# Kernel tuning notes

Measured on AMD Instinct MI355X. Metric: run time of the kernel, lower is better.

Reference implementation:

```python
import jax, jax.numpy as jnp
import numpy as np

N, K, D, H, DK, DV, L, E = 16384, 16, 128, 8, 16, 16, 2, 32
DFF = 4 * D
EPS = 1e-5


def _ln(x, g, b):
    mu = jnp.mean(x, axis=-1, keepdims=True)
    var = jnp.var(x, axis=-1, keepdims=True)
    return (x - mu) * jax.lax.rsqrt(var + EPS) * g + b


def setup_inputs() -> dict:
    key = jax.random.key(0)
    ks = jax.random.split(key, 20)
    inp = {
        "node_h": jax.random.normal(ks[0], (N, D), jnp.float32),
        "src_idx": jax.random.randint(ks[1], (N, K), 0, N),
        "edge_feat": jax.random.normal(ks[2], (N, K, E), jnp.float32),
        "t": jax.random.uniform(ks[3], (N, K), jnp.float32),
        "t_now": jnp.ones((1,), jnp.float32),
        # params (linear weights stored [in, out])
        "edge_fc_w": jax.random.normal(ks[4], (E, D), jnp.float32) * (2.0 / (E + D)) ** 0.5,
        "edge_fc_b": jnp.zeros((D,), jnp.float32),
        "basis_freq": jnp.asarray(1.0 / 10 ** np.linspace(0, 9, D), jnp.float32),
        "phase": jax.random.normal(ks[5], (D,), jnp.float32),
        "wq": jax.random.normal(ks[6], (L, D, H * DK), jnp.float32) * np.sqrt(2.0 / (D + DK)),
        "wk": jax.random.normal(ks[7], (L, D, H * DK), jnp.float32) * np.sqrt(2.0 / (D + DK)),
        "wv": jax.random.normal(ks[8], (L, D, H * DV), jnp.float32) * np.sqrt(2.0 / (D + DV)),
        "attn_fc_w": jax.random.normal(ks[9], (L, H * DV, D), jnp.float32) * (2.0 / (H * DV + D)) ** 0.5,
        "attn_fc_b": jnp.zeros((L, D), jnp.float32),
        "attn_ln_g": jnp.ones((L, D), jnp.float32),
        "attn_ln_b": jnp.zeros((L, D), jnp.float32),
        "ffn_w1": jax.random.normal(ks[10], (L, D, DFF), jnp.float32) * (1.0 / D) ** 0.5,
        "ffn_b1": jnp.zeros((L, DFF), jnp.float32),
        "ffn_w2": jax.random.normal(ks[11], (L, DFF, D), jnp.float32) * (1.0 / DFF) ** 0.5,
        "ffn_b2": jnp.zeros((L, D), jnp.float32),
        "ffn_ln_g": jnp.ones((L, D), jnp.float32),
        "ffn_ln_b": jnp.zeros((L, D), jnp.float32),
        "fea2node_w": jax.random.normal(ks[12], (D, D), jnp.float32) * (2.0 / (D + D)) ** 0.5,
        "fea2node_b": jnp.zeros((D,), jnp.float32),
        "final_ln_g": jnp.ones((D,), jnp.float32),
        "final_ln_b": jnp.zeros((D,), jnp.float32),
    }
    return inp


def reference(node_h, src_idx, edge_feat, t, t_now,
              edge_fc_w, edge_fc_b, basis_freq, phase,
              wq, wk, wv, attn_fc_w, attn_fc_b, attn_ln_g, attn_ln_b,
              ffn_w1, ffn_b1, ffn_w2, ffn_b2, ffn_ln_g, ffn_ln_b,
              fea2node_w, fea2node_b, final_ln_g, final_ln_b):
    scale = 1.0 / np.sqrt(DK).astype(np.float32)
    # message_func: gather src features, edge transform, temporal encoding
    t_enc = jnp.cos((t_now[0] - t)[..., None] * basis_freq + phase)        # [N,K,D]
    z = node_h[src_idx] + jax.nn.gelu(edge_feat @ edge_fc_w + edge_fc_b) + t_enc
    # reduce_func: inner_layer transformer blocks over the K-neighbor mailbox
    f = z
    for i in range(L):
        q = (f @ wq[i]).reshape(N, K, H, DK)
        k = (f @ wk[i]).reshape(N, K, H, DK)
        v = (f @ wv[i]).reshape(N, K, H, DV)
        attn = jax.nn.softmax(jnp.einsum('nqhd,nkhd->nhqk', q, k) * scale, axis=-1)
        out = jnp.einsum('nhqk,nkhd->nqhd', attn, v).reshape(N, K, H * DV)
        f = _ln(out @ attn_fc_w[i] + attn_fc_b[i] + f, attn_ln_g[i], attn_ln_b[i])
        hid = jax.nn.relu(f @ ffn_w1[i] + ffn_b1[i])                        # [N,K,4D]
        f = _ln(hid @ ffn_w2[i] + ffn_b2[i] + f, ffn_ln_g[i], ffn_ln_b[i])
    pooled = jnp.mean(f, axis=1)                                            # [N,D]
    out = _ln(jax.nn.gelu(pooled @ fea2node_w + fea2node_b) + node_h,
              final_ln_g, final_ln_b)
    return out
```

## Files before the change

### kernel.cpp

```cpp
#include <hip/hip_runtime.h>

#define NN 16384
#define OFF_EWT 0
#define OFF_WQT 4096
#define OFF_WKT 36864
#define OFF_WVT 69632
#define OFF_AFT 102400
#define OFF_W1T 135168
#define OFF_W2T 266240
#define OFF_F2N 397312
#define TOTAL_W 413696
#define FB_BYTE_OFF (1 << 20)

typedef __attribute__((ext_vector_type(8))) short bf16x8;
typedef __attribute__((ext_vector_type(4))) short bf16x4;
typedef __attribute__((ext_vector_type(4))) float f32x4;

static __device__ __forceinline__ short f2bf(float f) {
  unsigned u = __builtin_bit_cast(unsigned, f);
  u += 0x7fffu + ((u >> 16) & 1u);
  return (short)(u >> 16);
}
static __device__ __forceinline__ float bf2f(short h) {
  unsigned u = ((unsigned)(unsigned short)h) << 16;
  return __builtin_bit_cast(float, u);
}
static __device__ __forceinline__ float gelu_f(float x) {
  float e = __expf(1.5957691216057308f * (x + 0.044715f * x * x * x));
  return x - x / (e + 1.0f);
}
static __device__ __forceinline__ f32x4 mfma16(bf16x8 a, bf16x8 b, f32x4 c) {
  return __builtin_amdgcn_mfma_f32_16x16x32_bf16(a, b, c, 0, 0, 0);
}
#define SWZM(row) (((((row) & 7) << 4)) ^ ((((row) >> 3) & 3) << 5))
static __device__ __forceinline__ int swzb(int row, int col) {
  return row * 256 + ((col * 2) ^ SWZM(row));
}
static __device__ __forceinline__ bf16x8 tile_ld8(const short* base, int row, int col) {
  return *(const bf16x8*)((const char*)base + swzb(row, col));
}
static __device__ __forceinline__ void tile_st16(short* base, int row, int col, short v) {
  *(short*)((char*)base + swzb(row, col)) = v;
}
static __device__ __forceinline__ float tile_ldf(const short* base, int row, int col) {
  return bf2f(*(const short*)((const char*)base + swzb(row, col)));
}
static __device__ __forceinline__ void gll16(const short* sp, void* dstb) {
  __builtin_amdgcn_global_load_lds(
      (const __attribute__((address_space(1))) unsigned int*)sp,
      (__attribute__((address_space(3))) unsigned int*)dstb, 16, 0, 0);
}
static __device__ __forceinline__ void stage8(short* dst, const short* src, int stride,
                                              int w, int lane) {
  int dbase = w * 1024;
  int d = dbase + lane * 16;
  int row = d >> 8;
  int scolb = (d & 255) ^ SWZM(row);
  gll16(src + row * stride + (scolb >> 1), (char*)dst + dbase);
}
static __device__ __forceinline__ void stage_h8(short* dst, const short* src, int stride,
                                                int w, int lane) {
  #pragma unroll
  for (int it = 0; it < 2; ++it) {
    int dbase = (it * 8 + w) * 1024;
    int d = dbase + lane * 16;
    int row = d >> 8;
    int scolb = (d & 255) ^ SWZM(row);
    gll16(src + row * stride + (scolb >> 1), (char*)dst + dbase);
  }
}
static __device__ __forceinline__ void stage_f(short* dst, const short* src, int lane) {
  #pragma unroll
  for (int it = 0; it < 4; ++it) {
    int dbase = it * 1024;
    int d = dbase + lane * 16;
    int row = d >> 8;
    int scolb = (d & 255) ^ SWZM(row);
    gll16(src + row * 128 + (scolb >> 1), (char*)dst + dbase);
  }
}

#define LDS_FENCE() do {                                       \
    asm volatile("s_waitcnt lgkmcnt(0)" ::: "memory");         \
    __builtin_amdgcn_sched_barrier(0);                         \
  } while (0)

#define ENDSTEP() do {                                         \
    __syncthreads();                                           \
    short* _t = bc; bc = bn; bn = _t;                          \
  } while (0)

#define LD_FA(SRC)                                                        \
  _Pragma("unroll") for (int _s = 0; _s < 4; ++_s)                        \
      fA[_s] = tile_ld8((SRC), li, _s * 32 + lq * 8);

#define ST_TILE(T, ACC)                                                   \
  _Pragma("unroll") for (int _c = 0; _c < 8; ++_c)                        \
    _Pragma("unroll") for (int _r = 0; _r < 4; ++_r)                      \
      tile_st16((T), lq * 4 + _r, _c * 16 + li, f2bf((ACC)[_c][_r]));

#define PROJ1(BB)                                                         \
    f32x4 g0 = F0, g1 = F0;                                               \
    _Pragma("unroll") for (int _s = 0; _s < 4; ++_s) {                    \
      int _sc = _s * 32 + lq * 8;                                         \
      bf16x8 _b0 = tile_ld8((BB), 0 + li, _sc);                           \
      bf16x8 _b1 = tile_ld8((BB), 16 + li, _sc);                          \
      g0 = mfma16(fA[_s], _b0, g0);                                       \
      g1 = mfma16(fA[_s], _b1, g1);                                       \
    }

#define ST1(DST, CB)                                                      \
    _Pragma("unroll") for (int _r = 0; _r < 4; ++_r) {                    \
      tile_st16((DST), lq * 4 + _r, (CB) * 16 + li, f2bf(g0[_r]));        \
      tile_st16((DST), lq * 4 + _r, ((CB) + 1) * 16 + li, f2bf(g1[_r]));  \
    }

#define ACC1(AR, CB, BB)                                                  \
    _Pragma("unroll") for (int _s = 0; _s < 4; ++_s) {                    \
      int _sc = _s * 32 + lq * 8;                                         \
      bf16x8 _b0 = tile_ld8((BB), 0 + li, _sc);                           \
      bf16x8 _b1 = tile_ld8((BB), 16 + li, _sc);                          \
      acc[(CB)] = mfma16(AR[_s], _b0, acc[(CB)]);                         \
      acc[(CB) + 1] = mfma16(AR[_s], _b1, acc[(CB) + 1]);                 \
    }

#define PROJ4H(BB)                                                        \
    f32x4 g0 = F0, g1 = F0, g2 = F0, g3 = F0;                             \
    _Pragma("unroll") for (int _s = 0; _s < 4; ++_s) {                    \
      int _sc = _s * 32 + lq * 8;                                         \
      g0 = mfma16(fA[_s], tile_ld8((BB), 0 + li, _sc), g0);               \
      g1 = mfma16(fA[_s], tile_ld8((BB), 16 + li, _sc), g1);              \
      g2 = mfma16(fA[_s], tile_ld8((BB), 32 + li, _sc), g2);              \
      g3 = mfma16(fA[_s], tile_ld8((BB), 48 + li, _sc), g3);              \
    }

#define ACC4H(AR, CB, BB)                                                 \
    _Pragma("unroll") for (int _s = 0; _s < 4; ++_s) {                    \
      int _sc = _s * 32 + lq * 8;                                         \
      acc[(CB) + 0] = mfma16(AR[_s], tile_ld8((BB), 0 + li, _sc), acc[(CB) + 0]);  \
      acc[(CB) + 1] = mfma16(AR[_s], tile_ld8((BB), 16 + li, _sc), acc[(CB) + 1]); \
      acc[(CB) + 2] = mfma16(AR[_s], tile_ld8((BB), 32 + li, _sc), acc[(CB) + 2]); \
      acc[(CB) + 3] = mfma16(AR[_s], tile_ld8((BB), 48 + li, _sc), acc[(CB) + 3]); \
    }

#define LAYER_NORM(A, GP, BP) do {                                        \
    float _gg[8], _bb[8];                                                 \
    _Pragma("unroll") for (int _c = 0; _c < 8; ++_c) {                    \
      _gg[_c] = (GP)[_c * 16 + li]; _bb[_c] = (BP)[_c * 16 + li]; }       \
    _Pragma("unroll") for (int _r = 0; _r < 4; ++_r) {                    \
      float _s1 = 0.f, _s2 = 0.f;                                         \
      _Pragma("unroll") for (int _c = 0; _c < 8; ++_c) {                  \
        float _v = (A)[_c][_r]; _s1 += _v; _s2 += _v * _v; }              \
      _Pragma("unroll") for (int _m = 1; _m <= 8; _m <<= 1) {             \
        _s1 += __shfl_xor(_s1, _m, 64); _s2 += __shfl_xor(_s2, _m, 64); } \
      float _mean = _s1 * (1.f / 128.f);                                  \
      float _var = _s2 * (1.f / 128.f) - _mean * _mean;                   \
      float _rstd = rsqrtf(_var + 1e-5f);                                 \
      _Pragma("unroll") for (int _c = 0; _c < 8; ++_c)                    \
        (A)[_c][_r] = ((A)[_c][_r] - _mean) * _rstd * _gg[_c] + _bb[_c];  \
    }                                                                     \
  } while (0)

#define ATTN(MYQ, MYK, VACC, OA) do {                                     \
    f32x4 _st[8];                                                         \
    _Pragma("unroll") for (int _h = 0; _h < 8; ++_h) {                    \
      bf16x8 _ka = B0, _qa = B0;                                          \
      if (lq < 2) {                                                       \
        _ka = tile_ld8((MYK), li, _h * 16 + lq * 8);                      \
        _qa = tile_ld8((MYQ), li, _h * 16 + lq * 8);                      \
      }                                                                   \
      _st[_h] = mfma16(_ka, _qa, F0);                                     \
    }                                                                     \
    LDS_FENCE();                                                          \
    _Pragma("unroll") for (int _c = 0; _c < 8; ++_c) {                    \
      bf16x4 _pk;                                                         \
      _Pragma("unroll") for (int _r = 0; _r < 4; ++_r)                    \
        _pk[_r] = f2bf((VACC)[_c][_r]);                                   \
      *(bf16x4*)((MYK) + (_c * 16 + li) * 16 + lq * 4) = _pk;             \
    }                                                                     \
    LDS_FENCE();                                                          \
    _Pragma("unroll") for (int _h = 0; _h < 8; ++_h) {                    \
      float _p[4]; float _mx = -1e30f;                                    \
      _Pragma("unroll") for (int _r = 0; _r < 4; ++_r) {                  \
        _p[_r] = _st[_h][_r] * 0.25f; _mx = fmaxf(_mx, _p[_r]); }         \
      _mx = fmaxf(_mx, __shfl_xor(_mx, 16, 64));                          \
      _mx = fmaxf(_mx, __shfl_xor(_mx, 32, 64));                          \
      float _sum = 0.f;                                                   \
      _Pragma("unroll") for (int _r = 0; _r < 4; ++_r) {                  \
        _p[_r] = __expf(_p[_r] - _mx); _sum += _p[_r]; }                  \
      _sum += __shfl_xor(_sum, 16, 64);                                   \
      _sum += __shfl_xor(_sum, 32, 64);                                   \
      float _inv = 1.0f / _sum;                                           \
      _Pragma("unroll") for (int _r = 0; _r < 4; ++_r) _p[_r] *= _inv;    \
      bf16x8 _pa;                                                         \
      _Pragma("unroll") for (int _j = 0; _j < 8; ++_j) {                  \
        float _v = __shfl(_p[_j & 3], li + 16 * (2 * lq + (_j >> 2)), 64);\
        _pa[_j] = (lq < 2) ? f2bf(_v) : (short)0;                         \
      }                                                                   \
      bf16x8 _vb = B0;                                                    \
      if (lq < 2) _vb = *(const bf16x8*)((MYK) + (_h * 16 + li) * 16 + lq * 8); \
      f32x4 _o = mfma16(_pa, _vb, F0);                                    \
      _Pragma("unroll") for (int _r = 0; _r < 4; ++_r)                    \
        tile_st16((MYQ), lq * 4 + _r, _h * 16 + li, f2bf(_o[_r]));        \
    }                                                                     \
    LDS_FENCE();                                                          \
    _Pragma("unroll") for (int _s = 0; _s < 4; ++_s)                      \
      (OA)[_s] = tile_ld8((MYQ), li, _s * 32 + lq * 8);                   \
  } while (0)

__global__ void prep_kernel(const float* __restrict__ ew, const float* __restrict__ wq,
                            const float* __restrict__ wk, const float* __restrict__ wv,
                            const float* __restrict__ afc, const float* __restrict__ w1,
                            const float* __restrict__ w2, const float* __restrict__ f2n,
                            short* __restrict__ wsb) {
  int tt = blockIdx.x * 256 + threadIdx.x;
  if (tt >= TOTAL_W) return;
  short v;
  if (tt < OFF_WQT) {
    int u = tt; int row = u >> 5, colr = u & 31;
    v = f2bf(ew[colr * 128 + row]);
  } else if (tt < OFF_WKT) {
    int u = tt - OFF_WQT; int i = u >> 14; u &= 16383; int row = u >> 7, colr = u & 127;
    v = f2bf(wq[i * 16384 + colr * 128 + row]);
  } else if (tt < OFF_WVT) {
    int u = tt - OFF_WKT; int i = u >> 14; u &= 16383; int row = u >> 7, colr = u & 127;
    v = f2bf(wk[i * 16384 + colr * 128 + row]);
  } else if (tt < OFF_AFT) {
    int u = tt - OFF_WVT; int i = u >> 14; u &= 16383; int row = u >> 7, colr = u & 127;
    v = f2bf(wv[i * 16384 + colr * 128 + row]);
  } else if (tt < OFF_W1T) {
    int u = tt - OFF_AFT; int i = u >> 14; u &= 16383; int row = u >> 7, colr = u & 127;
    v = f2bf(afc[i * 16384 + colr * 128 + row]);
  } else if (tt < OFF_W2T) {
    int u = tt - OFF_W1T; int i = u >> 16; u &= 65535; int row = u >> 7, colr = u & 127;
    v = f2bf(w1[i * 65536 + colr * 512 + row]);
  } else if (tt < OFF_F2N) {
    int u = tt - OFF_W2T; int i = u >> 16; u &= 65535; int row = u >> 9, colr = u & 511;
    v = f2bf(w2[i * 65536 + colr * 128 + row]);
  } else {
    int u = tt - OFF_F2N; int row = u >> 7, colr = u & 127;
    v = f2bf(f2n[colr * 128 + row]);
  }
  wsb[tt] = v;
}

__global__ __launch_bounds__(512, 3) void attn_kernel(
    const float* __restrict__ node_h, const int* __restrict__ src_idx,
    const float* __restrict__ edge_feat, const float* __restrict__ t_arr,
    const float* __restrict__ t_now, const float* __restrict__ edge_fc_b,
    const float* __restrict__ basis_freq, const float* __restrict__ phase,
    const float* __restrict__ attn_fc_b, const float* __restrict__ attn_ln_g,
    const float* __restrict__ attn_ln_b, const short* __restrict__ wsb,
    short* __restrict__ fbuf, int il, int do_msg) {
  __shared__ __align__(16) short bufs0[4096];
  __shared__ __align__(16) short bufs1[4096];
  __shared__ __align__(16) short qk[8][4096];

  const int tid = (int)threadIdx.x;
  const int w = tid >> 6, lane = tid & 63, li = lane & 15, lq = lane >> 4;
  const int n = (int)blockIdx.x * 8 + w;
  short* myQ = qk[w];
  short* myK = qk[w] + 2048;
  short* bc = bufs0;
  short* bn = bufs1;
  const f32x4 F0 = {0.f, 0.f, 0.f, 0.f};
  const bf16x8 B0 = {0, 0, 0, 0, 0, 0, 0, 0};
  const short* WQT = wsb + OFF_WQT + il * 16384;
  const short* WKT = wsb + OFF_WKT + il * 16384;
  const short* WVT = wsb + OFF_WVT + il * 16384;
  const short* AFT = wsb + OFF_AFT + il * 16384;

  stage8(bc, WQT, 128, w, lane);

  f32x4 acc[8];
  if (do_msg) {
    const float tnow = t_now[0];
    {
      const float* ef = edge_feat + ((size_t)(n * 16 + li)) * 32 + lq * 8;
      f32x4 e0 = *(const f32x4*)(ef);
      f32x4 e1 = *(const f32x4*)(ef + 4);
      bf16x8 ea;
      #pragma unroll
      for (int j = 0; j < 4; ++j) { ea[j] = f2bf(e0[j]); ea[j + 4] = f2bf(e1[j]); }
      const short* ewt = wsb + OFF_EWT;
      #pragma unroll
      for (int c = 0; c < 8; ++c) {
        bf16x8 eb = *(const bf16x8*)(ewt + (c * 16 + li) * 32 + lq * 8);
        acc[c] = mfma16(ea, eb, F0);
      }
    }
    {
      float bfq[8], phs[8], ebs[8];
      #pragma unroll
      for (int c = 0; c < 8; ++c) {
        int col = c * 16 + li;
        bfq[c] = basis_freq[col]; phs[c] = phase[col]; ebs[c] = edge_fc_b[col];
      }
      #pragma unroll
      for (int r = 0; r < 4; ++r) {
        int m = lq * 4 + r;
        int sidx = src_idx[n * 16 + m];
        float dt = tnow - t_arr[n * 16 + m];
        const float* nh = node_h + (size_t)sidx * 128;
        #pragma unroll
        for (int c = 0; c < 8; ++c) {
          int col = c * 16 + li;
          float x = gelu_f(acc[c][r] + ebs[c]);
          x += nh[col];
          x += __cosf(dt * bfq[c] + phs[c]);
          acc[c][r] = x;
        }
      }
    }
    ST_TILE(myQ, acc);
  } else {
    stage_f(myQ, fbuf + (size_t)n * 2048, lane);
  }
  __syncthreads();
  if (!do_msg) {
    #pragma unroll
    for (int c = 0; c < 8; ++c)
      #pragma unroll
      for (int r = 0; r < 4; ++r)
        acc[c][r] = tile_ldf(myQ, lq * 4 + r, c * 16 + li);
  }

  bf16x8 fA[4], oa_[4];

  #pragma unroll
  for (int q = 0; q < 4; ++q) {
    const short* nx = (q < 3) ? (WQT + (q + 1) * 4096) : WKT;
    stage8(bn, nx, 128, w, lane);
    if (q == 0) LD_FA(myQ);
    { PROJ1(bc); ST1(myQ, q * 2); }
    ENDSTEP();
  }
  #pragma unroll
  for (int q = 0; q < 4; ++q) {
    const short* nx = (q < 3) ? (WKT + (q + 1) * 4096) : WVT;
    stage8(bn, nx, 128, w, lane);
    { PROJ1(bc); ST1(myK, q * 2); }
    ENDSTEP();
  }
  {
    f32x4 vacc[8];
    #pragma unroll
    for (int q = 0; q < 4; ++q) {
      const short* nx = (q < 3) ? (WVT + (q + 1) * 4096) : AFT;
      stage8(bn, nx, 128, w, lane);
      { PROJ1(bc); vacc[q * 2] = g0; vacc[q * 2 + 1] = g1; }
      if (q == 3) {
        LDS_FENCE();
        ATTN(myQ, myK, vacc, oa_);
      }
      ENDSTEP();
    }
  }
  #pragma unroll
  for (int q = 0; q < 4; ++q) {
    if (q < 3) stage8(bn, AFT + (q + 1) * 4096, 128, w, lane);
    #pragma unroll
    for (int j = 0; j < 2; ++j) {
      float b = attn_fc_b[il * 128 + (q * 2 + j) * 16 + li];
      #pragma unroll
      for (int r = 0; r < 4; ++r) acc[q * 2 + j][r] += b;
    }
    ACC1(oa_, q * 2, bc);
    if (q == 3) {
      LAYER_NORM(acc, attn_ln_g + il * 128, attn_ln_b + il * 128);
      ST_TILE(myQ, acc);
    }
    ENDSTEP();
  }
  LDS_FENCE();
  #pragma unroll
  for (int j = 0; j < 4; ++j) {
    int row = lane >> 2, colb = (lane & 3) * 32 + j * 8;
    bf16x8 v = tile_ld8(myQ, row, colb);
    *(bf16x8*)(fbuf + (size_t)n * 2048 + row * 128 + colb) = v;
  }
}

__global__ __launch_bounds__(512, 2) void ffn_kernel(
    const float* __restrict__ ffn_b1, const float* __restrict__ ffn_b2,
    const float* __restrict__ ffn_ln_g, const float* __restrict__ ffn_ln_b,
    const float* __restrict__ f2n_b, const float* __restrict__ fin_g,
    const float* __restrict__ fin_b, const float* __restrict__ node_h,
    const short* __restrict__ wsb, short* __restrict__ fbuf,
    float* __restrict__ out, int il, int last) {
  __shared__ __align__(16) short bufs0[8192];
  __shared__ __align__(16) short bufs1[8192];
  __shared__ __align__(16) short qk[8][2048];

  const int tid = (int)threadIdx.x;
  const int w = tid >> 6, lane = tid & 63, li = lane & 15, lq = lane >> 4;
  const int n = (int)blockIdx.x * 8 + w;
  short* myK = qk[w];
  short* bc = bufs0;
  short* bn = bufs1;
  const f32x4 F0 = {0.f, 0.f, 0.f, 0.f};
  const short* W1T = wsb + OFF_W1T + il * 65536;
  const short* W2T = wsb + OFF_W2T + il * 65536;

  stage_h8(bc, W1T, 128, w, lane);
  stage_f(myK, fbuf + (size_t)n * 2048, lane);
  __syncthreads();

  bf16x8 fA[4], ha_[4];
  LD_FA(myK);
  f32x4 acc[8];
  #pragma unroll
  for (int c = 0; c < 8; ++c) {
    float b2 = ffn_b2[il * 128 + c * 16 + li];
    #pragma unroll
    for (int r = 0; r < 4; ++r)
      acc[c][r] = tile_ldf(myK, lq * 4 + r, c * 16 + li) + b2;
  }
  LDS_FENCE();

  for (int ct = 0; ct < 4; ++ct) {
    const short* W1c = W1T + ct * 16384;
    const short* W2c = W2T + ct * 128;
    const float* b1p = ffn_b1 + il * 512 + ct * 128;
    #pragma unroll
    for (int h = 0; h < 2; ++h) {
      const short* nx = (h == 0) ? (W1c + 64 * 128) : W2c;
      stage_h8(bn, nx, (h == 0) ? 128 : 512, w, lane);
      {
        PROJ4H(bc);
        #pragma unroll
        for (int j = 0; j < 4; ++j) {
          float b1 = b1p[(h * 4 + j) * 16 + li];
          f32x4 gx = j == 0 ? g0 : j == 1 ? g1 : j == 2 ? g2 : g3;
          #pragma unroll
          for (int r = 0; r < 4; ++r)
            tile_st16(myK, lq * 4 + r, (h * 4 + j) * 16 + li, f2bf(fmaxf(gx[r] + b1, 0.f)));
        }
      }
      if (h == 1) {
        LDS_FENCE();
        #pragma unroll
        for (int s = 0; s < 4; ++s) ha_[s] = tile_ld8(myK, li, s * 32 + lq * 8);
      }
      ENDSTEP();
    }
    #pragma unroll
    for (int h = 0; h < 2; ++h) {
      if (h == 0) stage_h8(bn, W2c + 64 * 512, 512, w, lane);
      else if (ct < 3) stage_h8(bn, W1T + (ct + 1) * 16384, 128, w, lane);
      ACC4H(ha_, h * 4, bc);
      if (ct == 3 && h == 1)
        LAYER_NORM(acc, ffn_ln_g + il * 128, ffn_ln_b + il * 128);
      ENDSTEP();
    }
  }

  if (last) {
    float pc[8];
    #pragma unroll
    for (int c = 0; c < 8; ++c) {
      float s = acc[c][0] + acc[c][1] + acc[c][2] + acc[c][3];
      s += __shfl_xor(s, 16, 64);
      s += __shfl_xor(s, 32, 64);
      pc[c] = s * (1.f / 16.f);
    }
    float* ps = (float*)myK;
    if (lq == 0) {
      #pragma unroll
      for (int c = 0; c < 8; ++c) ps[c * 16 + li] = pc[c];
    }
    LDS_FENCE();
    const short* F2NT = wsb + OFF_F2N;
    float yv[2];
    #pragma unroll
    for (int half = 0; half < 2; ++half) {
      int col = half * 64 + lane;
      float dot = 0.f;
      for (int d0 = 0; d0 < 128; d0 += 8) {
        bf16x8 wv8 = *(const bf16x8*)(F2NT + col * 128 + d0);
        f32x4 p0 = *(const f32x4*)(ps + d0);
        f32x4 p1 = *(const f32x4*)(ps + d0 + 4);
        dot += p0[0] * bf2f(wv8[0]) + p0[1] * bf2f(wv8[1]) + p0[2] * bf2f(wv8[2]) + p0[3] * bf2f(wv8[3]);
        dot += p1[0] * bf2f(wv8[4]) + p1[1] * bf2f(wv8[5]) + p1[2] * bf2f(wv8[6]) + p1[3] * bf2f(wv8[7]);
      }
      yv[half] = gelu_f(dot + f2n_b[col]) + node_h[(size_t)n * 128 + col];
    }
    float s1 = yv[0] + yv[1], s2 = yv[0] * yv[0] + yv[1] * yv[1];
    #pragma unroll
    for (int m = 1; m <= 32; m <<= 1) { s1 += __shfl_xor(s1, m, 64); s2 += __shfl_xor(s2, m, 64); }
    float mean = s1 * (1.f / 128.f);
    float var = s2 * (1.f / 128.f) - mean * mean;
    float rstd = rsqrtf(var + 1e-5f);
    #pragma unroll
    for (int half = 0; half < 2; ++half) {
      int col = half * 64 + lane;
      out[(size_t)n * 128 + col] = (yv[half] - mean) * rstd * fin_g[col] + fin_b[col];
    }
  } else {
    ST_TILE(myK, acc);
    LDS_FENCE();
    #pragma unroll
    for (int j = 0; j < 4; ++j) {
      int row = lane >> 2, colb = (lane & 3) * 32 + j * 8;
      bf16x8 v = tile_ld8(myK, row, colb);
      *(bf16x8*)(fbuf + (size_t)n * 2048 + row * 128 + colb) = v;
    }
  }
}

extern "C" void kernel_launch(void* const* d_in, const int* in_sizes, int n_in,
                              void* d_out, int out_size, void* d_ws, size_t ws_size,
                              hipStream_t stream) {
  const float* node_h    = (const float*)d_in[0];
  const int*   src_idx   = (const int*)d_in[1];
  const float* edge_feat = (const float*)d_in[2];
  const float* t_arr     = (const float*)d_in[3];
  const float* t_now     = (const float*)d_in[4];
  const float* edge_fc_w = (const float*)d_in[5];
  const float* edge_fc_b = (const float*)d_in[6];
  const float* basis_frq = (const float*)d_in[7];
  const float* phase     = (const float*)d_in[8];
  const float* wq        = (const float*)d_in[9];
  const float* wk        = (const float*)d_in[10];
  const float* wv        = (const float*)d_in[11];
  const float* attn_fc_w = (const float*)d_in[12];
  const float* attn_fc_b = (const float*)d_in[13];
  const float* attn_ln_g = (const float*)d_in[14];
  const float* attn_ln_b = (const float*)d_in[15];
  const float* ffn_w1    = (const float*)d_in[16];
  const float* ffn_b1    = (const float*)d_in[17];
  const float* ffn_w2    = (const float*)d_in[18];
  const float* ffn_b2    = (const float*)d_in[19];
  const float* ffn_ln_g  = (const float*)d_in[20];
  const float* ffn_ln_b  = (const float*)d_in[21];
  const float* f2n_w     = (const float*)d_in[22];
  const float* f2n_b     = (const float*)d_in[23];
  const float* fin_g     = (const float*)d_in[24];
  const float* fin_b     = (const float*)d_in[25];
  short* wsb  = (short*)d_ws;
  short* fbuf = (short*)((char*)d_ws + FB_BYTE_OFF);

  prep_kernel<<<(TOTAL_W + 255) / 256, 256, 0, stream>>>(
      edge_fc_w, wq, wk, wv, attn_fc_w, ffn_w1, ffn_w2, f2n_w, wsb);
  attn_kernel<<<NN / 8, 512, 0, stream>>>(
      node_h, src_idx, edge_feat, t_arr, t_now, edge_fc_b, basis_frq, phase,
      attn_fc_b, attn_ln_g, attn_ln_b, wsb, fbuf, 0, 1);
  ffn_kernel<<<NN / 8, 512, 0, stream>>>(
      ffn_b1, ffn_b2, ffn_ln_g, ffn_ln_b, f2n_b, fin_g, fin_b, node_h,
      wsb, fbuf, (float*)d_out, 0, 0);
  attn_kernel<<<NN / 8, 512, 0, stream>>>(
      node_h, src_idx, edge_feat, t_arr, t_now, edge_fc_b, basis_frq, phase,
      attn_fc_b, attn_ln_g, attn_ln_b, wsb, fbuf, 1, 0);
  ffn_kernel<<<NN / 8, 512, 0, stream>>>(
      ffn_b1, ffn_b2, ffn_ln_g, ffn_ln_b, f2n_b, fin_g, fin_b, node_h,
      wsb, fbuf, (float*)d_out, 1, 1);
}
```

Baseline: 634.6 us.

## Process two nodes per wave in FFN using 32x32x16 MFMA tiles

The FFN kernel now has each wave handle two nodes (32 rows) and uses the 32x32x16 bf16 MFMA instead of 16x16x32. Each weight tile staged in LDS is therefore reused across twice as many rows, and the grid is halved. The LayerNorm moves after the loop and the epilogues are adapted to the 32-row accumulator layout. The trade-off is more accumulator registers and double the LDS per wave, which may reduce occupancy.

Result: slower. 803.9 us (+26.7%).

```diff
diff --git a/kernel.cpp b/kernel.cpp
--- a/kernel.cpp
+++ b/kernel.cpp
@@ -15,6 +15,7 @@
 typedef __attribute__((ext_vector_type(8))) short bf16x8;
 typedef __attribute__((ext_vector_type(4))) short bf16x4;
 typedef __attribute__((ext_vector_type(4))) float f32x4;
+typedef __attribute__((ext_vector_type(16))) float f32x16;
 
 static __device__ __forceinline__ short f2bf(float f) {
   unsigned u = __builtin_bit_cast(unsigned, f);
@@ -31,6 +32,9 @@
 }
 static __device__ __forceinline__ f32x4 mfma16(bf16x8 a, bf16x8 b, f32x4 c) {
   return __builtin_amdgcn_mfma_f32_16x16x32_bf16(a, b, c, 0, 0, 0);
+}
+static __device__ __forceinline__ f32x16 mfma32(bf16x8 a, bf16x8 b, f32x16 c) {
+  return __builtin_amdgcn_mfma_f32_32x32x16_bf16(a, b, c, 0, 0, 0);
 }
 #define SWZM(row) (((((row) & 7) << 4)) ^ ((((row) >> 3) & 3) << 5))
 static __device__ __forceinline__ int swzb(int row, int col) {
@@ -69,14 +73,16 @@
     gll16(src + row * stride + (scolb >> 1), (char*)dst + dbase);
   }
 }
-static __device__ __forceinline__ void stage_f(short* dst, const short* src, int lane) {
+static __device__ __forceinline__ void stage_f_ro(short* dst, const short* src, int lane,
+                                                  int ro) {
   #pragma unroll
   for (int it = 0; it < 4; ++it) {
     int dbase = it * 1024;
     int d = dbase + lane * 16;
-    int row = d >> 8;
+    int rl = d >> 8;
+    int row = ro + rl;
     int scolb = (d & 255) ^ SWZM(row);
-    gll16(src + row * 128 + (scolb >> 1), (char*)dst + dbase);
+    gll16(src + rl * 128 + (scolb >> 1), (char*)dst + ro * 256 + dbase);
   }
 }
 
@@ -122,25 +128,6 @@
       bf16x8 _b1 = tile_ld8((BB), 16 + li, _sc);                          \
       acc[(CB)] = mfma16(AR[_s], _b0, acc[(CB)]);                         \
       acc[(CB) + 1] = mfma16(AR[_s], _b1, acc[(CB) + 1]);                 \
-    }
-
-#define PROJ4H(BB)                                                        \
-    f32x4 g0 = F0, g1 = F0, g2 = F0, g3 = F0;                             \
-    _Pragma("unroll") for (int _s = 0; _s < 4; ++_s) {                    \
-      int _sc = _s * 32 + lq * 8;                                         \
-      g0 = mfma16(fA[_s], tile_ld8((BB), 0 + li, _sc), g0);               \
-      g1 = mfma16(fA[_s], tile_ld8((BB), 16 + li, _sc), g1);              \
-      g2 = mfma16(fA[_s], tile_ld8((BB), 32 + li, _sc), g2);              \
-      g3 = mfma16(fA[_s], tile_ld8((BB), 48 + li, _sc), g3);              \
-    }
-
-#define ACC4H(AR, CB, BB)                                                 \
-    _Pragma("unroll") for (int _s = 0; _s < 4; ++_s) {                    \
-      int _sc = _s * 32 + lq * 8;                                         \
-      acc[(CB) + 0] = mfma16(AR[_s], tile_ld8((BB), 0 + li, _sc), acc[(CB) + 0]);  \
-      acc[(CB) + 1] = mfma16(AR[_s], tile_ld8((BB), 16 + li, _sc), acc[(CB) + 1]); \
-      acc[(CB) + 2] = mfma16(AR[_s], tile_ld8((BB), 32 + li, _sc), acc[(CB) + 2]); \
-      acc[(CB) + 3] = mfma16(AR[_s], tile_ld8((BB), 48 + li, _sc), acc[(CB) + 3]); \
     }
 
 #define LAYER_NORM(A, GP, BP) do {                                        \
@@ -314,7 +301,7 @@
     }
     ST_TILE(myQ, acc);
   } else {
-    stage_f(myQ, fbuf + (size_t)n * 2048, lane);
+    stage_f_ro(myQ, fbuf + (size_t)n * 2048, lane, 0);
   }
   __syncthreads();
   if (!do_msg) {
@@ -390,31 +377,40 @@
     float* __restrict__ out, int il, int last) {
   __shared__ __align__(16) short bufs0[8192];
   __shared__ __align__(16) short bufs1[8192];
-  __shared__ __align__(16) short qk[8][2048];
+  __shared__ __align__(16) short tl[8][4096];
 
   const int tid = (int)threadIdx.x;
-  const int w = tid >> 6, lane = tid & 63, li = lane & 15, lq = lane >> 4;
-  const int n = (int)blockIdx.x * 8 + w;
-  short* myK = qk[w];
+  const int w = tid >> 6, lane = tid & 63, l31 = lane & 31, lh = lane >> 5;
+  const int n0 = (int)blockIdx.x * 16 + w * 2, n1 = n0 + 1;
+  short* myT = tl[w];
   short* bc = bufs0;
   short* bn = bufs1;
-  const f32x4 F0 = {0.f, 0.f, 0.f, 0.f};
   const short* W1T = wsb + OFF_W1T + il * 65536;
   const short* W2T = wsb + OFF_W2T + il * 65536;
+  f32x16 Z16;
+  #pragma unroll
+  for (int i = 0; i < 16; ++i) Z16[i] = 0.f;
 
   stage_h8(bc, W1T, 128, w, lane);
-  stage_f(myK, fbuf + (size_t)n * 2048, lane);
+  stage_f_ro(myT, fbuf + (size_t)n0 * 2048, lane, 0);
+  stage_f_ro(myT, fbuf + (size_t)n1 * 2048, lane, 16);
   __syncthreads();
 
-  bf16x8 fA[4], ha_[4];
-  LD_FA(myK);
-  f32x4 acc[8];
-  #pragma unroll
-  for (int c = 0; c < 8; ++c) {
-    float b2 = ffn_b2[il * 128 + c * 16 + li];
-    #pragma unroll
-    for (int r = 0; r < 4; ++r)
-      acc[c][r] = tile_ldf(myK, lq * 4 + r, c * 16 + li) + b2;
+  bf16x8 fA[8], ha[8];
+  #pragma unroll
+  for (int kc = 0; kc < 8; ++kc) fA[kc] = tile_ld8(myT, l31, kc * 16 + lh * 8);
+  f32x16 acc[4];
+  {
+    float b2v[4];
+    #pragma unroll
+    for (int t = 0; t < 4; ++t) b2v[t] = ffn_b2[il * 128 + t * 32 + l31];
+    #pragma unroll
+    for (int t = 0; t < 4; ++t)
+      #pragma unroll
+      for (int reg = 0; reg < 16; ++reg) {
+        int row = (reg & 3) + 8 * (reg >> 2) + 4 * lh;
+        acc[t][reg] = tile_ldf(myT, row, t * 32 + l31) + b2v[t];
+      }
   }
   LDS_FENCE();
 
@@ -427,20 +423,25 @@
       const short* nx = (h == 0) ? (W1c + 64 * 128) : W2c;
       stage_h8(bn, nx, (h == 0) ? 128 : 512, w, lane);
       {
-        PROJ4H(bc);
+        f32x16 g0 = Z16, g1 = Z16;
         #pragma unroll
-        for (int j = 0; j < 4; ++j) {
-          float b1 = b1p[(h * 4 + j) * 16 + li];
-          f32x4 gx = j == 0 ? g0 : j == 1 ? g1 : j == 2 ? g2 : g3;
-          #pragma unroll
-          for (int r = 0; r < 4; ++r)
-            tile_st16(myK, lq * 4 + r, (h * 4 + j) * 16 + li, f2bf(fmaxf(gx[r] + b1, 0.f)));
+        for (int kc = 0; kc < 8; ++kc) {
+          int kcol = kc * 16 + lh * 8;
+          g0 = mfma32(fA[kc], tile_ld8(bc, 0 + l31, kcol), g0);
+          g1 = mfma32(fA[kc], tile_ld8(bc, 32 + l31, kcol), g1);
+        }
+        float b10 = b1p[h * 64 + l31], b11 = b1p[h * 64 + 32 + l31];
+        #pragma unroll
+        for (int reg = 0; reg < 16; ++reg) {
+          int row = (reg & 3) + 8 * (reg >> 2) + 4 * lh;
+          tile_st16(myT, row, h * 64 + l31, f2bf(fmaxf(g0[reg] + b10, 0.f)));
+          tile_st16(myT, row, h * 64 + 32 + l31, f2bf(fmaxf(g1[reg] + b11, 0.f)));
         }
       }
       if (h == 1) {
         LDS_FENCE();
         #pragma unroll
-        for (int s = 0; s < 4; ++s) ha_[s] = tile_ld8(myK, li, s * 32 + lq * 8);
+        for (int kc = 0; kc < 8; ++kc) ha[kc] = tile_ld8(myT, l31, kc * 16 + lh * 8);
       }
       ENDSTEP();
     }
@@ -448,62 +449,109 @@
     for (int h = 0; h < 2; ++h) {
       if (h == 0) stage_h8(bn, W2c + 64 * 512, 512, w, lane);
       else if (ct < 3) stage_h8(bn, W1T + (ct + 1) * 16384, 128, w, lane);
-      ACC4H(ha_, h * 4, bc);
-      if (ct == 3 && h == 1)
-        LAYER_NORM(acc, ffn_ln_g + il * 128, ffn_ln_b + il * 128);
+      #pragma unroll
+      for (int kc = 0; kc < 8; ++kc) {
+        int kcol = kc * 16 + lh * 8;
+        acc[h * 2 + 0] = mfma32(ha[kc], tile_ld8(bc, 0 + l31, kcol), acc[h * 2 + 0]);
+        acc[h * 2 + 1] = mfma32(ha[kc], tile_ld8(bc, 32 + l31, kcol), acc[h * 2 + 1]);
+      }
       ENDSTEP();
     }
   }
 
+  {
+    float gg[4], bb[4];
+    #pragma unroll
+    for (int t = 0; t < 4; ++t) {
+      gg[t] = ffn_ln_g[il * 128 + t * 32 + l31];
+      bb[t] = ffn_ln_b[il * 128 + t * 32 + l31];
+    }
+    #pragma unroll
+    for (int reg = 0; reg < 16; ++reg) {
+      float s1 = 0.f, s2 = 0.f;
+      #pragma unroll
+      for (int t = 0; t < 4; ++t) { float v = acc[t][reg]; s1 += v; s2 += v * v; }
+      #pragma unroll
+      for (int m = 1; m <= 16; m <<= 1) {
+        s1 += __shfl_xor(s1, m, 64); s2 += __shfl_xor(s2, m, 64);
+      }
+      float mean = s1 * (1.f / 128.f);
+      float var = s2 * (1.f / 128.f) - mean * mean;
+      float rstd = rsqrtf(var + 1e-5f);
+      #pragma unroll
+      for (int t = 0; t < 4; ++t)
+        acc[t][reg] = (acc[t][reg] - mean) * rstd * gg[t] + bb[t];
+    }
+  }
+
   if (last) {
-    float pc[8];
-    #pragma unroll
-    for (int c = 0; c < 8; ++c) {
-      float s = acc[c][0] + acc[c][1] + acc[c][2] + acc[c][3];
-      s += __shfl_xor(s, 16, 64);
-      s += __shfl_xor(s, 32, 64);
-      pc[c] = s * (1.f / 16.f);
-    }
-    float* ps = (float*)myK;
-    if (lq == 0) {
-      #pragma unroll
-      for (int c = 0; c < 8; ++c) ps[c * 16 + li] = pc[c];
+    float pc0[4], pc1[4];
+    #pragma unroll
+    for (int t = 0; t < 4; ++t) {
+      float s0 = 0.f, s1v = 0.f;
+      #pragma unroll
+      for (int reg = 0; reg < 8; ++reg) { s0 += acc[t][reg]; s1v += acc[t][reg + 8]; }
+      s0 += __shfl_xor(s0, 32, 64);
+      s1v += __shfl_xor(s1v, 32, 64);
+      pc0[t] = s0 * (1.f / 16.f);
+      pc1[t] = s1v * (1.f / 16.f);
+    }
+    float* ps0 = (float*)myT;
+    float* ps1 = ps0 + 128;
+    if (lh == 0) {
+      #pragma unroll
+      for (int t = 0; t < 4; ++t) { ps0[t * 32 + l31] = pc0[t]; ps1[t * 32 + l31] = pc1[t]; }
     }
     LDS_FENCE();
     const short* F2NT = wsb + OFF_F2N;
-    float yv[2];
-    #pragma unroll
-    for (int half = 0; half < 2; ++half) {
-      int col = half * 64 + lane;
-      float dot = 0.f;
-      for (int d0 = 0; d0 < 128; d0 += 8) {
-        bf16x8 wv8 = *(const bf16x8*)(F2NT + col * 128 + d0);
-        f32x4 p0 = *(const f32x4*)(ps + d0);
-        f32x4 p1 = *(const f32x4*)(ps + d0 + 4);
-        dot += p0[0] * bf2f(wv8[0]) + p0[1] * bf2f(wv8[1]) + p0[2] * bf2f(wv8[2]) + p0[3] * bf2f(wv8[3]);
-        dot += p1[0] * bf2f(wv8[4]) + p1[1] * bf2f(wv8[5]) + p1[2] * bf2f(wv8[6]) + p1[3] * bf2f(wv8[7]);
-      }
-      yv[half] = gelu_f(dot + f2n_b[col]) + node_h[(size_t)n * 128 + col];
-    }
-    float s1 = yv[0] + yv[1], s2 = yv[0] * yv[0] + yv[1] * yv[1];
-    #pragma unroll
-    for (int m = 1; m <= 32; m <<= 1) { s1 += __shfl_xor(s1, m, 64); s2 += __shfl_xor(s2, m, 64); }
-    float mean = s1 * (1.f / 128.f);
-    float var = s2 * (1.f / 128.f) - mean * mean;
-    float rstd = rsqrtf(var + 1e-5f);
-    #pragma unroll
-    for (int half = 0; half < 2; ++half) {
-      int col = half * 64 + lane;
-      out[(size_t)n * 128 + col] = (yv[half] - mean) * rstd * fin_g[col] + fin_b[col];
+    #pragma unroll
+    for (int nd = 0; nd < 2; ++nd) {
+      const float* ps = nd ? ps1 : ps0;
+      int n = nd ? n1 : n0;
+      float yv[2];
+      #pragma unroll
+      for (int half = 0; half < 2; ++half) {
+        int col = half * 64 + lane;
+        float dot = 0.f;
+        for (int d0 = 0; d0 < 128; d0 += 8) {
+          bf16x8 wv8 = *(const bf16x8*)(F2NT + col * 128 + d0);
+          f32x4 p0 = *(const f32x4*)(ps + d0);
+          f32x4 p1 = *(const f32x4*)(ps + d0 + 4);
+          dot += p0[0] * bf2f(wv8[0]) + p0[1] * bf2f(wv8[1]) + p0[2] * bf2f(wv8[2]) + p0[3] * bf2f(wv8[3]);
+          dot += p1[0] * bf2f(wv8[4]) + p1[1] * bf2f(wv8[5]) + p1[2] * bf2f(wv8[6]) + p1[3] * bf2f(wv8[7]);
+        }
+        yv[half] = gelu_f(dot + f2n_b[col]) + node_h[(size_t)n * 128 + col];
+      }
+      float s1v = yv[0] + yv[1], s2v = yv[0] * yv[0] + yv[1] * yv[1];
+      #pragma unroll
+      for (int m = 1; m <= 32; m <<= 1) {
+        s1v += __shfl_xor(s1v, m, 64); s2v += __shfl_xor(s2v, m, 64);
+      }
+      float mean = s1v * (1.f / 128.f);
+      float var = s2v * (1.f / 128.f) - mean * mean;
+      float rstd = rsqrtf(var + 1e-5f);
+      #pragma unroll
+      for (int half = 0; half < 2; ++half) {
+        int col = half * 64 + lane;
+        out[(size_t)n * 128 + col] = (yv[half] - mean) * rstd * fin_g[col] + fin_b[col];
+      }
     }
   } else {
-    ST_TILE(myK, acc);
+    #pragma unroll
+    for (int t = 0; t < 4; ++t)
+      #pragma unroll
+      for (int reg = 0; reg < 16; ++reg) {
+        int row = (reg & 3) + 8 * (reg >> 2) + 4 * lh;
+        tile_st16(myT, row, t * 32 + l31, f2bf(acc[t][reg]));
+      }
     LDS_FENCE();
     #pragma unroll
-    for (int j = 0; j < 4; ++j) {
-      int row = lane >> 2, colb = (lane & 3) * 32 + j * 8;
-      bf16x8 v = tile_ld8(myK, row, colb);
-      *(bf16x8*)(fbuf + (size_t)n * 2048 + row * 128 + colb) = v;
+    for (int j = 0; j < 8; ++j) {
+      int chunk = j * 64 + lane;
+      int row = chunk >> 4, cole = (chunk & 15) * 8;
+      bf16x8 v = tile_ld8(myT, row, cole);
+      int n = (row >> 4) ? n1 : n0;
+      *(bf16x8*)(fbuf + (size_t)n * 2048 + (row & 15) * 128 + cole) = v;
     }
   }
 }
@@ -545,13 +593,13 @@
   attn_kernel<<<NN / 8, 512, 0, stream>>>(
       node_h, src_idx, edge_feat, t_arr, t_now, edge_fc_b, basis_frq, phase,
       attn_fc_b, attn_ln_g, attn_ln_b, wsb, fbuf, 0, 1);
-  ffn_kernel<<<NN / 8, 512, 0, stream>>>(
+  ffn_kernel<<<NN / 16, 512, 0, stream>>>(
       ffn_b1, ffn_b2, ffn_ln_g, ffn_ln_b, f2n_b, fin_g, fin_b, node_h,
       wsb, fbuf, (float*)d_out, 0, 0);
   attn_kernel<<<NN / 8, 512, 0, stream>>>(
       node_h, src_idx, edge_feat, t_arr, t_now, edge_fc_b, basis_frq, phase,
       attn_fc_b, attn_ln_g, attn_ln_b, wsb, fbuf, 1, 0);
-  ffn_kernel<<<NN / 8, 512, 0, stream>>>(
+  ffn_kernel<<<NN / 16, 512, 0, stream>>>(
       ffn_b1, ffn_b2, ffn_ln_g, ffn_ln_b, f2n_b, fin_g, fin_b, node_h,
       wsb, fbuf, (float*)d_out, 1, 1);
 }
```
